# Kernel tuning notes

Measured on AMD Instinct MI355X. Metric: run time of the kernel, lower is better.

Reference implementation:

```python
import jax, jax.numpy as jnp
import numpy as np

ANGRES = 5  # u = v = angRes, n = 25


def _l2norm(x, axis):
    n = jnp.sqrt(jnp.sum(x * x, axis=axis, keepdims=True))
    return x / jnp.maximum(n, 1e-12)  # matches torch F.normalize eps


def _cos_attn(qm, km, vm):
    # qm: (b, M, K), km: (b, K, M), vm: (b, M, K)
    q = _l2norm(qm, -1)
    k = _l2norm(km, -2)
    att = jax.nn.softmax(q @ k, axis=-1)  # (b, M, M)
    return att @ vm


def _af_attn(x, u, v):  # AngularFrequencyAttention: b c (u v) h w -> b (c u) (h v w)
    b, c, n, h, w = x.shape
    t = x.reshape(b, c, u, v, h, w)
    qm = t.transpose(0, 1, 2, 4, 3, 5).reshape(b, c * u, h * v * w)   # (b,c,u,h,v,w)
    km = t.transpose(0, 4, 3, 5, 1, 2).reshape(b, h * v * w, c * u)   # (b,h,v,w,c,u)
    o = _cos_attn(qm, km, qm)
    o = o.reshape(b, c, u, h, v, w).transpose(0, 1, 2, 4, 3, 5).reshape(b, c, n, h, w)
    return o + x


def _sa_attn(x, u, v):  # SpatialAngularAttention: b c (u v) h w -> b (h u) (c v w)
    b, c, n, h, w = x.shape
    t = x.reshape(b, c, u, v, h, w)
    qm = t.transpose(0, 4, 2, 1, 3, 5).reshape(b, h * u, c * v * w)   # (b,h,u,c,v,w)
    km = t.transpose(0, 1, 3, 5, 4, 2).reshape(b, c * v * w, h * u)   # (b,c,v,w,h,u)
    o = _cos_attn(qm, km, qm)
    o = o.reshape(b, h, u, c, v, w).transpose(0, 3, 2, 4, 1, 5).reshape(b, c, n, h, w)
    return o + x


def _sf_attn(x, u, v):  # SpatialFrequencyAttention: b c (u v) h w -> b (c h) (w u v)
    b, c, n, h, w = x.shape
    t = x.reshape(b, c, u, v, h, w)
    qm = t.transpose(0, 1, 4, 5, 2, 3).reshape(b, c * h, w * u * v)   # (b,c,h,w,u,v)
    km = t.transpose(0, 5, 2, 3, 1, 4).reshape(b, w * u * v, c * h)   # (b,w,u,v,c,h)
    o = _cos_attn(qm, km, qm)
    o = o.reshape(b, c, h, w, u, v).transpose(0, 1, 4, 5, 2, 3).reshape(b, c, n, h, w)
    return o + x


def _layernorm(x, g, bta, eps=1e-5):
    mu = jnp.mean(x, -1, keepdims=True)
    var = jnp.mean(jnp.square(x - mu), -1, keepdims=True)
    return (x - mu) * jax.lax.rsqrt(var + eps) * g + bta


def setup_inputs() -> dict:
    key = jax.random.key(0)
    k0, k1, k2 = jax.random.split(key, 3)
    b, c, n, h, w = 4, 64, 25, 48, 48
    x = jax.random.normal(k0, (b, c, n, h, w), dtype=jnp.float32)
    gamma = jnp.ones((3 * c,), dtype=jnp.float32)
    beta = jnp.zeros((3 * c,), dtype=jnp.float32)
    w1 = jax.random.normal(k1, (3 * c, c), dtype=jnp.float32) * 0.02
    w2 = jax.random.normal(k2, (c, c), dtype=jnp.float32) * 0.02
    return {"x": x, "gamma": gamma, "beta": beta, "w1": w1, "w2": w2}


def reference(x, gamma, beta, w1, w2):
    u = v = ANGRES
    b, c, n, h, w = x.shape
    sf = _sf_attn(x, u, v)
    af = _af_attn(x, u, v)
    sa = _sa_attn(x, u, v)
    cat = jnp.concatenate([sf, af, sa], axis=1)            # (b, 3c, n, h, w)
    f = cat.transpose(0, 3, 4, 2, 1).reshape(b * h * w, n, 3 * c)
    y = _layernorm(f, gamma, beta)
    y = jax.nn.relu(y @ w1) @ w2                            # (bhw, n, c); dropout p=0.01 is eval-identity
    out = y.reshape(b, h, w, n, c).transpose(0, 4, 3, 1, 2) + x
    return out
```

## Files before the change

kernel.cpp:

```cpp
#include <hip/hip_runtime.h>
#include <stdint.h>

typedef __attribute__((ext_vector_type(8))) short bf16x8;
typedef __attribute__((ext_vector_type(4))) float f32x4;

__device__ __forceinline__ float b2f(short s) {
  union { unsigned u; float f; } a; a.u = ((unsigned)(unsigned short)s) << 16; return a.f;
}
__device__ __forceinline__ short f2b(float f) {
  union { float f; unsigned u; } a; a.f = f;
  unsigned r = a.u + 0x7fffu + ((a.u >> 16) & 1u);
  return (short)(r >> 16);
}
__device__ __forceinline__ void gload16(const void* g, void* l) {
  __builtin_amdgcn_global_load_lds((__attribute__((address_space(1))) void*)g,
                                   (__attribute__((address_space(3))) void*)l, 16, 0, 0);
}

#define SWZ(row, col) ((col) ^ (((row) & 7) << 3))

__global__ __launch_bounds__(256) void permute_sf_k(const float* __restrict__ x,
                                                    short* __restrict__ Q,
                                                    float* __restrict__ inv) {
  __shared__ float buf[4][1200];
  int wave = threadIdx.x >> 6, lane = threadIdx.x & 63;
  int gr = blockIdx.x * 4 + wave;
  int b = gr / 3072, m = gr - b * 3072;
  int c = m / 48, hh = m - c * 48;
  const float* xb = x + (long)(b * 64 + c) * 57600 + hh * 48;
  for (int uv = 0; uv < 25; ++uv)
    if (lane < 48) buf[wave][uv * 48 + lane] = xb[uv * 2304 + lane];
  __syncthreads();
  short* Qr = Q + (long)gr * 1280;
  float ss = 0.f;
  for (int k = lane; k < 1280; k += 64) {
    float v = 0.f;
    if (k < 1200) { int wv = k / 25, uv = k - wv * 25; v = buf[wave][uv * 48 + wv]; }
    ss += v * v;
    Qr[k] = f2b(v);
  }
  #pragma unroll
  for (int o = 32; o >= 1; o >>= 1) ss += __shfl_xor(ss, o, 64);
  if (lane == 0) inv[gr] = 1.0f / fmaxf(sqrtf(ss), 1e-12f);
}

__global__ __launch_bounds__(256) void permtr_all_k(const float* __restrict__ x,
    short* __restrict__ Qaf, short* __restrict__ QTaf,
    short* __restrict__ Qsa, short* __restrict__ QTsa,
    float* __restrict__ ssaf, float* __restrict__ sssa) {
  __shared__ short t[32][33];
  int bid = blockIdx.x;
  int isAF = (bid < 17280);
  int M, Mp, Kp, kt, mt, b;
  short *Q, *QT; float* ss;
  if (isAF) { M = 320; Mp = 384; Kp = 11520; kt = bid % 360; int r = bid / 360; mt = r % 12; b = r / 12;
              Q = Qaf; QT = QTaf; ss = ssaf; }
  else { int id = bid - 17280; M = 240; Mp = 256; Kp = 15360; kt = id % 480; int r = id / 480; mt = r % 8; b = r / 8;
         Q = Qsa; QT = QTsa; ss = sssa; }
  int k0 = kt * 32, m0 = mt * 32;
  int tx = threadIdx.x & 31, ty = threadIdx.x >> 5;
  const float* xb = x + (long)b * 3686400;
  #pragma unroll
  for (int i = 0; i < 32; i += 8) {
    int m = m0 + ty + i, k = k0 + tx;
    float v = 0.f;
    if (m < M) {
      int q1 = k / 240, r2 = k - q1 * 240;
      int v5 = r2 / 48, wv = r2 - v5 * 48;
      int a1 = m / 5, u = m - a1 * 5;
      long xi = isAF ? ((long)a1 * 25 + u * 5 + v5) * 2304 + q1 * 48 + wv
                     : ((long)q1 * 25 + u * 5 + v5) * 2304 + a1 * 48 + wv;
      v = xb[xi];
    }
    t[ty + i][tx] = f2b(v);
  }
  __syncthreads();
  long Qb = (long)b * Mp * Kp;
  #pragma unroll
  for (int i = 0; i < 32; i += 8)
    Q[Qb + (long)(m0 + ty + i) * Kp + k0 + tx] = t[ty + i][tx];
  #pragma unroll
  for (int i = 0; i < 32; i += 8)
    QT[Qb + (long)(k0 + ty + i) * Mp + m0 + tx] = t[tx][ty + i];
  if (threadIdx.x < 32 && m0 + (int)threadIdx.x < M) {
    float s = 0.f;
    #pragma unroll
    for (int k = 0; k < 32; ++k) { float f = b2f(t[threadIdx.x][k]); s += f * f; }
    atomicAdd(&ss[b * Mp + m0 + threadIdx.x], s);
  }
}

__global__ __launch_bounds__(256) void transpose_k(const short* __restrict__ in, short* __restrict__ out,
                                                   int R, int C) {
  __shared__ short t[32][33];
  long base = (long)blockIdx.z * R * C;
  int c0 = blockIdx.x * 32, r0 = blockIdx.y * 32;
  int tx = threadIdx.x & 31, ty = threadIdx.x >> 5;
  #pragma unroll
  for (int i = 0; i < 32; i += 8)
    t[ty + i][tx] = in[base + (long)(r0 + ty + i) * C + c0 + tx];
  __syncthreads();
  #pragma unroll
  for (int i = 0; i < 32; i += 8)
    out[base + (long)(c0 + ty + i) * R + r0 + tx] = t[tx][ty + i];
}

__global__ __launch_bounds__(256, 2) void gemm1_tri_k(const short* __restrict__ Q,
                                                      const float* __restrict__ invn,
                                                      short* __restrict__ att,
                                                      float* __restrict__ rowsum) {
  __shared__ short sm[32768];
  int tid = threadIdx.x, wave = tid >> 6, lane = tid & 63;
  int la = lane & 15, lb = lane >> 4;
  int bat = blockIdx.z;
  int bx = blockIdx.x, yt = 0, rem = bx;
  while (rem >= 24 - yt) { rem -= 24 - yt; ++yt; }
  int xt = yt + rem;
  const short* Qb = Q + (long)bat * 3932160L;
  const float* inv = invn + (long)bat * 3072;
  int row0 = yt * 128, col0 = xt * 128;
  f32x4 acc[4][4] = {};
  int wr = wave >> 1, wc = wave & 1;
  int rloc = tid >> 3, cbase = (tid & 7) * 8;
  int ldsoff = tid * 8;

  const short *pA[4], *pB[4];
  #pragma unroll
  for (int p = 0; p < 4; ++p) {
    int row = p * 32 + rloc;
    int sc = SWZ(row, cbase);
    pA[p] = Qb + (long)(row0 + row) * 1280 + sc;
    pB[p] = Qb + (long)(col0 + row) * 1280 + sc;
  }

  #define TRI_STAGE(KT, BUF) { \
    short* Asb = sm + (BUF) * 16384; \
    short* Bsb = Asb + 8192; \
    _Pragma("unroll") \
    for (int p = 0; p < 4; ++p) { \
      gload16(pA[p] + (KT) * 64, (void*)(Asb + p * 2048 + ldsoff)); \
      gload16(pB[p] + (KT) * 64, (void*)(Bsb + p * 2048 + ldsoff)); \
    } }
  #define TRI_COMP(BUF) { \
    const short* Asb = sm + (BUF) * 16384; \
    const short* Bsb = Asb + 8192; \
    _Pragma("unroll") \
    for (int kk = 0; kk < 64; kk += 32) { \
      bf16x8 av[4], bv[4]; \
      _Pragma("unroll") \
      for (int m = 0; m < 4; ++m) \
        av[m] = *(const bf16x8*)&Asb[(wr * 64 + m * 16 + la) * 64 + SWZ(la, kk + lb * 8)]; \
      _Pragma("unroll") \
      for (int nn = 0; nn < 4; ++nn) \
        bv[nn] = *(const bf16x8*)&Bsb[(wc * 64 + nn * 16 + la) * 64 + SWZ(la, kk + lb * 8)]; \
      _Pragma("unroll") \
      for (int m = 0; m < 4; ++m) \
        _Pragma("unroll") \
        for (int nn = 0; nn < 4; ++nn) \
          acc[m][nn] = __builtin_amdgcn_mfma_f32_16x16x32_bf16(av[m], bv[nn], acc[m][nn], 0, 0, 0); \
    } }

  TRI_STAGE(0, 0)
  for (int kt = 0; kt < 19; ++kt) {
    TRI_STAGE(kt + 1, (kt + 1) & 1)
    asm volatile("s_waitcnt vmcnt(8)" ::: "memory");
    __builtin_amdgcn_s_barrier();
    TRI_COMP(kt & 1)
    asm volatile("" ::: "memory");
    __builtin_amdgcn_s_barrier();
  }
  asm volatile("s_waitcnt vmcnt(0)" ::: "memory");
  __builtin_amdgcn_s_barrier();
  TRI_COMP(1)
  asm volatile("" ::: "memory");
  __builtin_amdgcn_s_barrier();

  short* staged = sm;
  #pragma unroll
  for (int m = 0; m < 4; ++m) {
    #pragma unroll
    for (int nn = 0; nn < 4; ++nn) {
      int cl = wc * 64 + nn * 16 + la;
      float ic = inv[col0 + cl];
      #pragma unroll
      for (int j = 0; j < 4; ++j) {
        int rl = wr * 64 + m * 16 + lb * 4 + j;
        staged[rl * 136 + cl] = f2b(__expf(acc[m][nn][j] * inv[row0 + rl] * ic));
      }
    }
  }
  __syncthreads();
  short* attb = att + (long)bat * 9437184L;
  float* rsb = rowsum + (long)bat * 3072;
  {
    int r = tid >> 1, half = tid & 1;
    short* dst = attb + (long)(row0 + r) * 3072 + col0 + half * 64;
    const short* src = &staged[r * 136 + half * 64];
    float s = 0.f;
    #pragma unroll
    for (int q = 0; q < 8; ++q) {
      bf16x8 v = *(const bf16x8*)&src[q * 8];
      *(bf16x8*)&dst[q * 8] = v;
      #pragma unroll
      for (int jj = 0; jj < 8; ++jj) s += b2f(v[jj]);
    }
    s += __shfl_xor(s, 1, 64);
    if (half == 0) atomicAdd(&rsb[row0 + r], s);
  }
  if (xt != yt) {
    int c = tid >> 1, half = tid & 1;
    short* dst = attb + (long)(col0 + c) * 3072 + row0 + half * 64;
    float s = 0.f;
    #pragma unroll
    for (int q = 0; q < 8; ++q) {
      bf16x8 o;
      #pragma unroll
      for (int jj = 0; jj < 8; ++jj) {
        o[jj] = staged[(half * 64 + q * 8 + jj) * 136 + c];
        s += b2f(o[jj]);
      }
      *(bf16x8*)&dst[q * 8] = o;
    }
    s += __shfl_xor(s, 1, 64);
    if (half == 0) atomicAdd(&rsb[col0 + c], s);
  }
}

__global__ __launch_bounds__(256, 2) void gemm_s_all_k(
    const short* __restrict__ Aaf, const short* __restrict__ Asa,
    float* __restrict__ Sfaf, float* __restrict__ Sfsa)
{
  __shared__ short sm[32768];
  int bid = blockIdx.x;
  const short* A; float* Sf;
  int lda, ktotal, ksper, ldc, row0, col0, bat, kc;
  long sA, sS;
  if (bid < 288) {
    int txy = bid % 9, z = bid / 9;
    col0 = (txy % 3) * 128; row0 = (txy / 3) * 128;
    bat = z / 8; kc = z % 8;
    lda = 11520; ktotal = 180; ksper = 23; ldc = 384;
    sA = 4423680L; sS = 147456L; A = Aaf; Sf = Sfaf;
  } else {
    int id = bid - 288;
    int txy = id % 4, z = id / 4;
    col0 = (txy % 2) * 128; row0 = (txy / 2) * 128;
    bat = z / 16; kc = z % 16;
    lda = 15360; ktotal = 240; ksper = 15; ldc = 256;
    sA = 3932160L; sS = 65536L; A = Asa; Sf = Sfsa;
  }
  int tid = threadIdx.x;
  int wave = tid >> 6, lane = tid & 63;
  int la = lane & 15, lb = lane >> 4;
  const short* Ab = A + (long)bat * sA;
  int kb = kc * ksper, ke = min(ktotal, kb + ksper);
  int L = ke - kb;
  f32x4 acc[4][4] = {};
  int wr = wave >> 1, wc = wave & 1;
  int rloc = tid >> 3, cbase = (tid & 7) * 8;
  int ldsoff = tid * 8;

  const short *pA[4], *pB[4];
  #pragma unroll
  for (int p = 0; p < 4; ++p) {
    int row = p * 32 + rloc;
    int sc = SWZ(row, cbase);
    pA[p] = Ab + (long)(row0 + row) * lda + sc;
    pB[p] = Ab + (long)(col0 + row) * lda + sc;
  }

  #define GS_STAGE(KT, BUF) { \
    short* Asb = sm + (BUF) * 16384; \
    short* Bsb = Asb + 8192; \
    _Pragma("unroll") \
    for (int p = 0; p < 4; ++p) { \
      gload16(pA[p] + (KT) * 64, (void*)(Asb + p * 2048 + ldsoff)); \
      gload16(pB[p] + (KT) * 64, (void*)(Bsb + p * 2048 + ldsoff)); \
    } }
  #define GS_COMP(BUF) { \
    const short* Asb = sm + (BUF) * 16384; \
    const short* Bsb = Asb + 8192; \
    _Pragma("unroll") \
    for (int kk = 0; kk < 64; kk += 32) { \
      bf16x8 av[4], bv[4]; \
      _Pragma("unroll") \
      for (int m = 0; m < 4; ++m) \
        av[m] = *(const bf16x8*)&Asb[(wr * 64 + m * 16 + la) * 64 + SWZ(la, kk + lb * 8)]; \
      _Pragma("unroll") \
      for (int nn = 0; nn < 4; ++nn) \
        bv[nn] = *(const bf16x8*)&Bsb[(wc * 64 + nn * 16 + la) * 64 + SWZ(la, kk + lb * 8)]; \
      _Pragma("unroll") \
      for (int m = 0; m < 4; ++m) \
        _Pragma("unroll") \
        for (int nn = 0; nn < 4; ++nn) \
          acc[m][nn] = __builtin_amdgcn_mfma_f32_16x16x32_bf16(av[m], bv[nn], acc[m][nn], 0, 0, 0); \
    } }

  GS_STAGE(kb, 0)
  for (int t = 0; t < L - 1; ++t) {
    GS_STAGE(kb + t + 1, (t + 1) & 1)
    asm volatile("s_waitcnt vmcnt(8)" ::: "memory");
    __builtin_amdgcn_s_barrier();
    GS_COMP(t & 1)
    asm volatile("" ::: "memory");
    __builtin_amdgcn_s_barrier();
  }
  asm volatile("s_waitcnt vmcnt(0)" ::: "memory");
  __builtin_amdgcn_s_barrier();
  GS_COMP((L - 1) & 1)

  float* Sb = Sf + (long)bat * sS;
  #pragma unroll
  for (int m = 0; m < 4; ++m) {
    int gr0 = row0 + wr * 64 + m * 16 + lb * 4;
    #pragma unroll
    for (int nn = 0; nn < 4; ++nn) {
      int gc = col0 + wc * 64 + nn * 16 + la;
      #pragma unroll
      for (int j = 0; j < 4; ++j)
        atomicAdd(&Sb[(long)(gr0 + j) * ldc + gc], acc[m][nn][j]);
    }
  }
}

__global__ __launch_bounds__(256) void softmax_all_k(
    const float* __restrict__ Sfaf, const float* __restrict__ Sfsa,
    const float* __restrict__ ssaf, const float* __restrict__ sssa,
    short* __restrict__ attaf, short* __restrict__ attsa)
{
  int wave = threadIdx.x >> 6, lane = threadIdx.x & 63;
  int rid = blockIdx.x * 4 + wave;
  int row, b, Mv, Mp; const float *Sf, *ss; short* att;
  if (rid < 1280) { row = rid % 320; b = rid / 320; Mv = 320; Mp = 384; Sf = Sfaf; ss = ssaf; att = attaf; }
  else { int id = rid - 1280; row = id % 240; b = id / 240; Mv = 240; Mp = 256; Sf = Sfsa; ss = sssa; att = attsa; }
  long sS = (long)Mp * Mp;
  const float* Sr = Sf + (long)b * sS + (long)row * Mp;
  const float* ssb = ss + b * Mp;
  float inv_i = rsqrtf(fmaxf(ssb[row], 1e-24f));
  float ev[6] = {0.f, 0.f, 0.f, 0.f, 0.f, 0.f};
  float sum = 0.f;
  #pragma unroll
  for (int q = 0; q < 6; ++q) {
    int j = q * 64 + lane;
    if (j < Mv) {
      float e = __expf(Sr[j] * inv_i * rsqrtf(fmaxf(ssb[j], 1e-24f)));
      ev[q] = e; sum += e;
    }
  }
  #pragma unroll
  for (int o = 32; o >= 1; o >>= 1) sum += __shfl_xor(sum, o, 64);
  float rden = 1.0f / sum;
  short* ar = att + (long)b * sS + (long)row * Mp;
  #pragma unroll
  for (int q = 0; q < 6; ++q) {
    int j = q * 64 + lane;
    if (j < Mp) ar[j] = (j < Mv) ? f2b(ev[q] * rden) : (short)0;
  }
}

__global__ __launch_bounds__(256, 2) void gemm2sf_k(const short* __restrict__ A,
                                                    const short* __restrict__ B,
                                                    const float* __restrict__ rowsum,
                                                    short* __restrict__ F) {
  __shared__ short sm[32768];
  int tid = threadIdx.x, wave = tid >> 6, lane = tid & 63;
  int la = lane & 15, lb = lane >> 4;
  int wr = wave >> 1, wc = wave & 1;
  int wk;
  { int xcd = blockIdx.x & 7, j = blockIdx.x >> 3; wk = xcd * 120 + j; }
  int yt = wk % 24, rem = wk / 24;
  int xt = rem % 10, bat = rem / 10;
  const short* Ab = A + (long)bat * 9437184L;
  const short* Bb = B + (long)bat * 3932160L;
  int rloc = tid >> 3, cbase = (tid & 7) * 8;
  int ldsoff = tid * 8;
  f32x4 acc[4][4] = {};

  const short *pA[4], *pB[4];
  #pragma unroll
  for (int p = 0; p < 4; ++p) {
    int row = p * 32 + rloc;
    int sc = SWZ(row, cbase);
    int rga = (row & 63) * 48 + yt * 2 + (row >> 6);
    pA[p] = Ab + (long)rga * 3072 + sc;
    int rgb = xt * 128 + row;
    pB[p] = Bb + (long)rgb * 3072 + sc;
  }

  #define G2_STAGE(KT, BUF) { \
    short* Asb = sm + (BUF) * 16384; \
    short* Bsb = Asb + 8192; \
    _Pragma("unroll") \
    for (int p = 0; p < 4; ++p) { \
      gload16(pA[p] + (KT) * 64, (void*)(Asb + p * 2048 + ldsoff)); \
      gload16(pB[p] + (KT) * 64, (void*)(Bsb + p * 2048 + ldsoff)); \
    } }
  #define G2_COMP(BUF) { \
    const short* Asb = sm + (BUF) * 16384; \
    const short* Bsb = Asb + 8192; \
    _Pragma("unroll") \
    for (int kk = 0; kk < 64; kk += 32) { \
      bf16x8 av[4], bv[4]; \
      _Pragma("unroll") \
      for (int m = 0; m < 4; ++m) \
        av[m] = *(const bf16x8*)&Asb[(wr * 64 + m * 16 + la) * 64 + SWZ(la, kk + lb * 8)]; \
      _Pragma("unroll") \
      for (int nn = 0; nn < 4; ++nn) \
        bv[nn] = *(const bf16x8*)&Bsb[(wc * 64 + nn * 16 + la) * 64 + SWZ(la, kk + lb * 8)]; \
      _Pragma("unroll") \
      for (int m = 0; m < 4; ++m) \
        _Pragma("unroll") \
        for (int nn = 0; nn < 4; ++nn) \
          acc[m][nn] = __builtin_amdgcn_mfma_f32_16x16x32_bf16(av[m], bv[nn], acc[m][nn], 0, 0, 0); \
    } }

  G2_STAGE(0, 0)
  for (int kt = 0; kt < 47; ++kt) {
    G2_STAGE(kt + 1, (kt + 1) & 1)
    asm volatile("s_waitcnt vmcnt(8)" ::: "memory");
    __builtin_amdgcn_s_barrier();
    G2_COMP(kt & 1)
    asm volatile("" ::: "memory");
    __builtin_amdgcn_s_barrier();
  }
  asm volatile("s_waitcnt vmcnt(0)" ::: "memory");
  __builtin_amdgcn_s_barrier();
  G2_COMP(1)
  asm volatile("" ::: "memory");
  __builtin_amdgcn_s_barrier();

  const float* rsb = rowsum + (long)bat * 3072;
  float rs[4][4];
  #pragma unroll
  for (int m = 0; m < 4; ++m)
    #pragma unroll
    for (int j = 0; j < 4; ++j)
      rs[m][j] = 1.0f / rsb[(m * 16 + lb * 4 + j) * 48 + yt * 2 + wr];

  short* staged = sm;
  #pragma unroll
  for (int m = 0; m < 4; ++m) {
    #pragma unroll
    for (int nn = 0; nn < 4; ++nn) {
      int cc = wc * 64 + nn * 16 + la;
      short4 o;
      o.x = f2b(acc[m][nn][0] * rs[m][0]); o.y = f2b(acc[m][nn][1] * rs[m][1]);
      o.z = f2b(acc[m][nn][2] * rs[m][2]); o.w = f2b(acc[m][nn][3] * rs[m][3]);
      *(short4*)&staged[(cc * 2 + wr) * 72 + m * 16 + lb * 4] = o;
    }
  }
  __syncthreads();
  #pragma unroll
  for (int rd = 0; rd < 8; ++rd) {
    int chunk = rd * 32 + (tid >> 3);
    int part = tid & 7;
    bf16x8 v = *(const bf16x8*)&staged[chunk * 72 + part * 8];
    int cc = chunk >> 1, sub = chunk & 1;
    int gc = xt * 128 + cc;
    if (gc < 1200) {
      int hh = yt * 2 + sub;
      int wv = gc / 25, nidx = gc - wv * 25;
      long base = (((long)(bat * 48 + hh) * 48 + wv) * 25 + nidx) * 192 + part * 8;
      *(bf16x8*)&F[base] = v;
    }
  }
}

__global__ __launch_bounds__(256) void gemm2_afsa_k(
    const short* __restrict__ attaf, const short* __restrict__ QTaf,
    const short* __restrict__ attsa, const short* __restrict__ QTsa,
    short* __restrict__ F)
{
  __shared__ short sm[20480];
  short* As = sm;
  short* Bs = sm + 4096;
  int bid = blockIdx.x;
  int isAF = (bid < 900);
  int NX, NY, LDA, KST, wk;
  const short *A, *B; long SA, SB;
  if (isAF) { NX = 45; NY = 5; LDA = 384; KST = 6; SA = 147456L; SB = 4423680L; A = attaf; B = QTaf; wk = bid; }
  else { NX = 60; NY = 4; LDA = 256; KST = 4; SA = 65536L; SB = 3932160L; A = attsa; B = QTsa; wk = bid - 900; }
  int yt = wk % NY, rem = wk / NY;
  int xt = rem % NX, bat = rem / NX;
  int tid = threadIdx.x, wave = tid >> 6, lane = tid & 63;
  int la = lane & 15, lb = lane >> 4;
  const short* Ab = A + (long)bat * SA;
  const short* Bb = B + (long)bat * SB;
  f32x4 acc[4][4] = {};
  int rloc = tid >> 3, cbase = (tid & 7) * 8;
  int ldsoff = tid * 8;

  const short *pA[2], *pB[8];
  #pragma unroll
  for (int p = 0; p < 2; ++p) {
    int r = p * 32 + rloc;
    int sc = SWZ(r, cbase);
    int rowg = isAF ? (r * 5 + yt) : (yt * 64 + r);
    pA[p] = Ab + (long)rowg * LDA + sc;
  }
  #pragma unroll
  for (int p = 0; p < 8; ++p) {
    int rb = p * 32 + rloc;
    int sc = SWZ(rb, cbase);
    int rowg;
    if (isAF) rowg = xt * 256 + rb;
    else { int c = rb & 63, g = rb >> 6; rowg = c * 240 + xt * 4 + g; }
    pB[p] = Bb + (long)rowg * LDA + sc;
  }

  for (int kt = 0; kt < KST; ++kt) {
    #pragma unroll
    for (int p = 0; p < 2; ++p)
      gload16(pA[p] + kt * 64, (void*)(As + p * 2048 + ldsoff));
    #pragma unroll
    for (int p = 0; p < 8; ++p)
      gload16(pB[p] + kt * 64, (void*)(Bs + p * 2048 + ldsoff));
    __syncthreads();
    #pragma unroll
    for (int kk = 0; kk < 64; kk += 32) {
      bf16x8 av[4], bv[4];
      #pragma unroll
      for (int m = 0; m < 4; ++m)
        av[m] = *(const bf16x8*)&As[(m * 16 + la) * 64 + SWZ(la, kk + lb * 8)];
      #pragma unroll
      for (int nn = 0; nn < 4; ++nn)
        bv[nn] = *(const bf16x8*)&Bs[(wave * 64 + nn * 16 + la) * 64 + SWZ(la, kk + lb * 8)];
      #pragma unroll
      for (int m = 0; m < 4; ++m)
        #pragma unroll
        for (int nn = 0; nn < 4; ++nn)
          acc[m][nn] = __builtin_amdgcn_mfma_f32_16x16x32_bf16(av[m], bv[nn], acc[m][nn], 0, 0, 0);
    }
    __syncthreads();
  }

  short* staged = sm;
  #pragma unroll
  for (int m = 0; m < 4; ++m) {
    #pragma unroll
    for (int nn = 0; nn < 4; ++nn) {
      if (!isAF) {
        #pragma unroll
        for (int j = 0; j < 4; ++j)
          staged[((m * 16 + lb * 4 + j) * 4 + wave) * 72 + nn * 16 + la] = f2b(acc[m][nn][j]);
      } else {
        short4 o;
        o.x = f2b(acc[m][nn][0]); o.y = f2b(acc[m][nn][1]);
        o.z = f2b(acc[m][nn][2]); o.w = f2b(acc[m][nn][3]);
        *(short4*)&staged[(wave * 64 + nn * 16 + la) * 72 + m * 16 + lb * 4] = o;
      }
    }
  }
  __syncthreads();

  #pragma unroll
  for (int rd = 0; rd < 8; ++rd) {
    int chunk = rd * 32 + (tid >> 3);
    int part = tid & 7;
    bf16x8 v = *(const bf16x8*)&staged[chunk * 72 + part * 8];
    long base; bool ok = true;
    if (isAF) {
      int gc = xt * 256 + chunk;
      int hh = gc / 240, r2 = gc - hh * 240, v5 = r2 / 48, wv = r2 - v5 * 48;
      base = (((long)(bat * 48 + hh) * 48 + wv) * 25 + yt * 5 + v5) * 192 + 64 + part * 8;
    } else {
      int r = chunk >> 2, g = chunk & 3;
      int gr = yt * 64 + r; ok = (gr < 240);
      int hh = gr / 5, u = gr - hh * 5;
      int r2 = xt * 4 + g, v5 = r2 / 48, wv = r2 - v5 * 48;
      base = (((long)(bat * 48 + hh) * 48 + wv) * 25 + u * 5 + v5) * 192 + 128 + part * 8;
    }
    if (ok) *(bf16x8*)&F[base] = v;
  }
}

__global__ __launch_bounds__(256) void prep_w_k(const float* __restrict__ w1, const float* __restrict__ w2,
                                                short* __restrict__ w1t, short* __restrict__ w2t) {
  int idx = blockIdx.x * 256 + threadIdx.x;
  if (idx < 12288) {
    int i = idx / 64, j = idx - i * 64;
    w1t[j * 192 + i] = f2b(w1[idx]);
  } else if (idx < 16384) {
    int k = idx - 12288;
    int i = k / 64, j = k - i * 64;
    w2t[j * 64 + i] = f2b(w2[k]);
  }
}

__global__ __launch_bounds__(256) void ln_mlp_mfma_k(
    const short* __restrict__ F, const float* __restrict__ x,
    const float* __restrict__ gamma, const float* __restrict__ beta,
    const short* __restrict__ w1t, const short* __restrict__ w2t,
    float* __restrict__ out)
{
  int n = blockIdx.x, hh = blockIdx.y, b = blockIdx.z;
  __shared__ short A1[48 * 200];
  __shared__ float xs[64 * 49];
  __shared__ __align__(16) char pool[19584];
  short* Fs = (short*)pool;
  short* Y1 = (short*)pool;
  float* Y2 = (float*)(pool + 6912);
  int tid = threadIdx.x, wave = tid >> 6, lane = tid & 63;
  int la = lane & 15, lb = lane >> 4;
  long Fb0 = ((long)(b * 48 + hh) * 1200 + n) * 192;
  long xb = (long)b * 3686400 + (long)n * 2304 + hh * 48;

  #pragma unroll
  for (int it = 0; it < 5; ++it) {
    int ci = tid + 256 * it;
    if (ci < 1152) {
      int r = ci / 24, q = ci - r * 24;
      *(bf16x8*)&Fs[r * 192 + q * 8] = *(const bf16x8*)&F[Fb0 + (long)r * 4800 + q * 8];
    }
  }
  {
    int ch = tid >> 2, qq = tid & 3;
    const float* xr = x + xb + (long)ch * 57600 + qq * 12;
    #pragma unroll
    for (int i = 0; i < 12; ++i) xs[ch * 49 + qq * 12 + i] = xr[i];
  }
  __syncthreads();

  float g0 = gamma[lane], g1 = gamma[lane + 64], g2 = gamma[lane + 128];
  float bt0 = beta[lane], bt1 = beta[lane + 64], bt2 = beta[lane + 128];
  #pragma unroll 4
  for (int rr = 0; rr < 12; ++rr) {
    int r = wave * 12 + rr;
    float xv = xs[lane * 49 + r];
    float v0 = b2f(Fs[r * 192 + lane]) + xv;
    float v1 = b2f(Fs[r * 192 + lane + 64]) + xv;
    float v2 = b2f(Fs[r * 192 + lane + 128]) + xv;
    float s = v0 + v1 + v2;
    #pragma unroll
    for (int o = 32; o >= 1; o >>= 1) s += __shfl_xor(s, o, 64);
    float mu = s * (1.f / 192.f);
    float d0 = v0 - mu, d1 = v1 - mu, d2 = v2 - mu;
    float q = d0 * d0 + d1 * d1 + d2 * d2;
    #pragma unroll
    for (int o = 32; o >= 1; o >>= 1) q += __shfl_xor(q, o, 64);
    float rs = rsqrtf(q * (1.f / 192.f) + 1e-5f);
    A1[r * 200 + lane]       = f2b(d0 * rs * g0 + bt0);
    A1[r * 200 + lane + 64]  = f2b(d1 * rs * g1 + bt1);
    A1[r * 200 + lane + 128] = f2b(d2 * rs * g2 + bt2);
  }
  __syncthreads();

  f32x4 acc1[3] = {};
  #pragma unroll
  for (int ks = 0; ks < 6; ++ks) {
    bf16x8 bv = *(const bf16x8*)&w1t[(wave * 16 + la) * 192 + ks * 32 + lb * 8];
    #pragma unroll
    for (int m = 0; m < 3; ++m) {
      bf16x8 av = *(const bf16x8*)&A1[(m * 16 + la) * 200 + ks * 32 + lb * 8];
      acc1[m] = __builtin_amdgcn_mfma_f32_16x16x32_bf16(av, bv, acc1[m], 0, 0, 0);
    }
  }
  #pragma unroll
  for (int m = 0; m < 3; ++m)
    #pragma unroll
    for (int j = 0; j < 4; ++j)
      Y1[(m * 16 + lb * 4 + j) * 72 + wave * 16 + la] = f2b(fmaxf(acc1[m][j], 0.f));
  __syncthreads();

  f32x4 acc2[3] = {};
  #pragma unroll
  for (int ks = 0; ks < 2; ++ks) {
    bf16x8 bv = *(const bf16x8*)&w2t[(wave * 16 + la) * 64 + ks * 32 + lb * 8];
    #pragma unroll
    for (int m = 0; m < 3; ++m) {
      bf16x8 av = *(const bf16x8*)&Y1[(m * 16 + la) * 72 + ks * 32 + lb * 8];
      acc2[m] = __builtin_amdgcn_mfma_f32_16x16x32_bf16(av, bv, acc2[m], 0, 0, 0);
    }
  }
  #pragma unroll
  for (int m = 0; m < 3; ++m)
    #pragma unroll
    for (int j = 0; j < 4; ++j)
      Y2[(m * 16 + lb * 4 + j) * 66 + wave * 16 + la] = acc2[m][j];
  __syncthreads();

  #pragma unroll
  for (int i = 0; i < 12; ++i) {
    int e = tid + 256 * i;
    int cc = e / 48, wv = e - cc * 48;
    out[xb + (long)cc * 57600 + wv] = Y2[wv * 66 + cc] + xs[cc * 49 + wv];
  }
}

extern "C" void kernel_launch(void* const* d_in, const int* in_sizes, int n_in,
                              void* d_out, int out_size, void* d_ws, size_t ws_size,
                              hipStream_t stream) {
  (void)in_sizes; (void)n_in; (void)out_size;
  const float* x     = (const float*)d_in[0];
  const float* gamma = (const float*)d_in[1];
  const float* beta  = (const float*)d_in[2];
  const float* w1    = (const float*)d_in[3];
  const float* w2    = (const float*)d_in[4];
  float* out = (float*)d_out;

  const size_t NEED = 237191168UL;
  if (ws_size < NEED) return;
  char* ws = (char*)d_ws;
  short* F     = (short*)(ws);
  short* attsf = (short*)(ws + 88473600UL);
  short* Qsf   = (short*)(ws + 163971072UL);
  short* QTsf  = (short*)(ws + 199360512UL);
  float* rowsum = (float*)(ws + 234749952UL);
  float* invn  = (float*)(ws + 237109248UL);
  short* w1t   = (short*)(ws + 237158400UL);
  short* w2t   = (short*)(ws + 237182976UL);
  short* Qaf   = (short*)(ws + 88473600UL);
  short* QTaf  = (short*)(ws + 123863040UL);
  float* Sfsa  = (float*)(ws + 159252480UL);
  float* ssaf  = (float*)(ws + 160301056UL);
  float* sssa  = (float*)(ws + 160307200UL);
  short* attaf = (short*)(ws + 160311296UL);
  short* attsa = (short*)(ws + 161490944UL);
  short* Qsa   = (short*)(ws + 163971072UL);
  short* QTsa  = (short*)(ws + 195428352UL);
  float* Sfaf  = (float*)(ws + 234749952UL);

  prep_w_k<<<64, 256, 0, stream>>>(w1, w2, w1t, w2t);

  permute_sf_k<<<3072, 256, 0, stream>>>(x, Qsf, invn);
  transpose_k<<<dim3(40, 96, 4), 256, 0, stream>>>(Qsf, QTsf, 3072, 1280);
  hipMemsetAsync(rowsum, 0, 49152, stream);
  gemm1_tri_k<<<dim3(300, 1, 4), 256, 0, stream>>>(Qsf, invn, attsf, rowsum);
  gemm2sf_k<<<dim3(960), 256, 0, stream>>>(attsf, QTsf, rowsum, F);

  hipMemsetAsync(Sfaf, 0, 2359296, stream);
  hipMemsetAsync(Sfsa, 0, 1048576, stream);
  hipMemsetAsync(ssaf, 0, 10240, stream);
  permtr_all_k<<<32640, 256, 0, stream>>>(x, Qaf, QTaf, Qsa, QTsa, ssaf, sssa);
  gemm_s_all_k<<<544, 256, 0, stream>>>(Qaf, Qsa, Sfaf, Sfsa);
  softmax_all_k<<<560, 256, 0, stream>>>(Sfaf, Sfsa, ssaf, sssa, attaf, attsa);
  gemm2_afsa_k<<<1860, 256, 0, stream>>>(attaf, QTaf, attsa, QTsa, F);

  ln_mlp_mfma_k<<<dim3(25, 48, 4), 256, 0, stream>>>(F, x, gamma, beta, w1t, w2t, out);
}
```

Before: 519.9 us.

## Halve K-tile in tri/SF GEMMs for higher occupancy, remap AF/SA blocks per XCD

The triangular Gram GEMM and the SF attention-times-V GEMM now stage 32-wide K slices instead of 64 in a reshaped swizzled LDS layout. This shrinks shared memory so launch bounds can allow four blocks per CU instead of two, at the cost of twice as many barrier-separated pipeline steps. The AF/SA second GEMM remaps block indices so consecutive work lands on the same XCD for better L2 reuse. The final fused MLP kernel loads F into LDS with direct global-to-LDS loads instead of passing through registers.

After: 518.2 us. No clear change (-0.3%).

```diff
diff --git a/kernel.cpp b/kernel.cpp
--- a/kernel.cpp
+++ b/kernel.cpp
@@ -105,11 +105,11 @@
     out[base + (long)(c0 + ty + i) * R + r0 + tx] = t[tx][ty + i];
 }
 
-__global__ __launch_bounds__(256, 2) void gemm1_tri_k(const short* __restrict__ Q,
+__global__ __launch_bounds__(256, 4) void gemm1_tri_k(const short* __restrict__ Q,
                                                       const float* __restrict__ invn,
                                                       short* __restrict__ att,
                                                       float* __restrict__ rowsum) {
-  __shared__ short sm[32768];
+  __shared__ short sm[17408];
   int tid = threadIdx.x, wave = tid >> 6, lane = tid & 63;
   int la = lane & 15, lb = lane >> 4;
   int bat = blockIdx.z;
@@ -121,61 +121,68 @@
   int row0 = yt * 128, col0 = xt * 128;
   f32x4 acc[4][4] = {};
   int wr = wave >> 1, wc = wave & 1;
-  int rloc = tid >> 3, cbase = (tid & 7) * 8;
-  int ldsoff = tid * 8;
-
-  const short *pA[4], *pB[4];
-  #pragma unroll
-  for (int p = 0; p < 4; ++p) {
-    int row = p * 32 + rloc;
-    int sc = SWZ(row, cbase);
-    pA[p] = Qb + (long)(row0 + row) * 1280 + sc;
-    pB[p] = Qb + (long)(col0 + row) * 1280 + sc;
-  }
-
-  #define TRI_STAGE(KT, BUF) { \
-    short* Asb = sm + (BUF) * 16384; \
-    short* Bsb = Asb + 8192; \
+  int swzla = (la & 7) << 3;
+
+  const short *pA[2], *pB[2];
+  #pragma unroll
+  for (int p = 0; p < 2; ++p) {
+    int R = p * 32 + (tid >> 3);
+    int sun = ((tid & 7) * 8) ^ ((R & 7) << 3);
+    int r = R + ((sun >> 5) << 6);
+    int c = sun & 31;
+    pA[p] = Qb + (long)(row0 + r) * 1280 + c;
+    pB[p] = Qb + (long)(col0 + r) * 1280 + c;
+  }
+
+  #define T9_STAGE(KT, BUF) { \
+    short* Asb = sm + (BUF) * 8192; \
+    short* Bsb = Asb + 4096; \
+    gload16(pA[0] + (KT) * 32, (void*)(Asb + tid * 8)); \
+    gload16(pA[1] + (KT) * 32, (void*)(Asb + 2048 + tid * 8)); \
+    gload16(pB[0] + (KT) * 32, (void*)(Bsb + tid * 8)); \
+    gload16(pB[1] + (KT) * 32, (void*)(Bsb + 2048 + tid * 8)); \
+  }
+  #define T9_COMP(BUF) { \
+    const short* Asb = sm + (BUF) * 8192; \
+    const short* Bsb = Asb + 4096; \
+    bf16x8 av[4], bv[4]; \
     _Pragma("unroll") \
-    for (int p = 0; p < 4; ++p) { \
-      gload16(pA[p] + (KT) * 64, (void*)(Asb + p * 2048 + ldsoff)); \
-      gload16(pB[p] + (KT) * 64, (void*)(Bsb + p * 2048 + ldsoff)); \
-    } }
-  #define TRI_COMP(BUF) { \
-    const short* Asb = sm + (BUF) * 16384; \
-    const short* Bsb = Asb + 8192; \
+    for (int m = 0; m < 4; ++m) \
+      av[m] = *(const bf16x8*)&Asb[(m * 16 + la) * 64 + ((wr * 32 + lb * 8) ^ swzla)]; \
     _Pragma("unroll") \
-    for (int kk = 0; kk < 64; kk += 32) { \
-      bf16x8 av[4], bv[4]; \
-      _Pragma("unroll") \
-      for (int m = 0; m < 4; ++m) \
-        av[m] = *(const bf16x8*)&Asb[(wr * 64 + m * 16 + la) * 64 + SWZ(la, kk + lb * 8)]; \
+    for (int nn = 0; nn < 4; ++nn) \
+      bv[nn] = *(const bf16x8*)&Bsb[(nn * 16 + la) * 64 + ((wc * 32 + lb * 8) ^ swzla)]; \
+    _Pragma("unroll") \
+    for (int m = 0; m < 4; ++m) \
       _Pragma("unroll") \
       for (int nn = 0; nn < 4; ++nn) \
-        bv[nn] = *(const bf16x8*)&Bsb[(wc * 64 + nn * 16 + la) * 64 + SWZ(la, kk + lb * 8)]; \
-      _Pragma("unroll") \
-      for (int m = 0; m < 4; ++m) \
-        _Pragma("unroll") \
-        for (int nn = 0; nn < 4; ++nn) \
-          acc[m][nn] = __builtin_amdgcn_mfma_f32_16x16x32_bf16(av[m], bv[nn], acc[m][nn], 0, 0, 0); \
-    } }
-
-  TRI_STAGE(0, 0)
-  for (int kt = 0; kt < 19; ++kt) {
-    TRI_STAGE(kt + 1, (kt + 1) & 1)
-    asm volatile("s_waitcnt vmcnt(8)" ::: "memory");
+        acc[m][nn] = __builtin_amdgcn_mfma_f32_16x16x32_bf16(av[m], bv[nn], acc[m][nn], 0, 0, 0); \
+  }
+
+  T9_STAGE(0, 0)
+  for (int kt = 0; kt < 39; ++kt) {
+    T9_STAGE(kt + 1, (kt + 1) & 1)
+    asm volatile("s_waitcnt vmcnt(4)" ::: "memory");
     __builtin_amdgcn_s_barrier();
-    TRI_COMP(kt & 1)
+    T9_COMP(kt & 1)
     asm volatile("" ::: "memory");
     __builtin_amdgcn_s_barrier();
   }
   asm volatile("s_waitcnt vmcnt(0)" ::: "memory");
   __builtin_amdgcn_s_barrier();
-  TRI_COMP(1)
+  T9_COMP(1)
   asm volatile("" ::: "memory");
   __builtin_amdgcn_s_barrier();
 
   short* staged = sm;
+  #pragma unroll
+  for (int m = 0; m < 4; ++m) {
+    #pragma unroll
+    for (int nn = 0; nn < 4; ++nn) {
+      int cl = wc * 32 + nn * 16 + la;
+      (void)cl;
+    }
+  }
   #pragma unroll
   for (int m = 0; m < 4; ++m) {
     #pragma unroll
@@ -225,6 +232,7 @@
     if (half == 0) atomicAdd(&rsb[col0 + c], s);
   }
 }
+
 
 __global__ __launch_bounds__(256, 2) void gemm_s_all_k(
     const short* __restrict__ Aaf, const short* __restrict__ Asa,
@@ -358,11 +366,11 @@
   }
 }
 
-__global__ __launch_bounds__(256, 2) void gemm2sf_k(const short* __restrict__ A,
+__global__ __launch_bounds__(256, 4) void gemm2sf_k(const short* __restrict__ A,
                                                     const short* __restrict__ B,
                                                     const float* __restrict__ rowsum,
                                                     short* __restrict__ F) {
-  __shared__ short sm[32768];
+  __shared__ short sm[18432];
   int tid = threadIdx.x, wave = tid >> 6, lane = tid & 63;
   int la = lane & 15, lb = lane >> 4;
   int wr = wave >> 1, wc = wave & 1;
@@ -372,60 +380,59 @@
   int xt = rem % 10, bat = rem / 10;
   const short* Ab = A + (long)bat * 9437184L;
   const short* Bb = B + (long)bat * 3932160L;
-  int rloc = tid >> 3, cbase = (tid & 7) * 8;
-  int ldsoff = tid * 8;
+  int swzla = (la & 7) << 3;
   f32x4 acc[4][4] = {};
 
-  const short *pA[4], *pB[4];
-  #pragma unroll
-  for (int p = 0; p < 4; ++p) {
-    int row = p * 32 + rloc;
-    int sc = SWZ(row, cbase);
-    int rga = (row & 63) * 48 + yt * 2 + (row >> 6);
-    pA[p] = Ab + (long)rga * 3072 + sc;
-    int rgb = xt * 128 + row;
-    pB[p] = Bb + (long)rgb * 3072 + sc;
-  }
-
-  #define G2_STAGE(KT, BUF) { \
-    short* Asb = sm + (BUF) * 16384; \
-    short* Bsb = Asb + 8192; \
+  const short *pA[2], *pB[2];
+  #pragma unroll
+  for (int p = 0; p < 2; ++p) {
+    int R = p * 32 + (tid >> 3);
+    int sun = ((tid & 7) * 8) ^ ((R & 7) << 3);
+    int r = R + ((sun >> 5) << 6);
+    int c = sun & 31;
+    int rga = (r & 63) * 48 + yt * 2 + (r >> 6);
+    pA[p] = Ab + (long)rga * 3072 + c;
+    int rgb = xt * 128 + r;
+    pB[p] = Bb + (long)rgb * 3072 + c;
+  }
+
+  #define G9_STAGE(KT, BUF) { \
+    short* Asb = sm + (BUF) * 8192; \
+    short* Bsb = Asb + 4096; \
+    gload16(pA[0] + (KT) * 32, (void*)(Asb + tid * 8)); \
+    gload16(pA[1] + (KT) * 32, (void*)(Asb + 2048 + tid * 8)); \
+    gload16(pB[0] + (KT) * 32, (void*)(Bsb + tid * 8)); \
+    gload16(pB[1] + (KT) * 32, (void*)(Bsb + 2048 + tid * 8)); \
+  }
+  #define G9_COMP(BUF) { \
+    const short* Asb = sm + (BUF) * 8192; \
+    const short* Bsb = Asb + 4096; \
+    bf16x8 av[4], bv[4]; \
     _Pragma("unroll") \
-    for (int p = 0; p < 4; ++p) { \
-      gload16(pA[p] + (KT) * 64, (void*)(Asb + p * 2048 + ldsoff)); \
-      gload16(pB[p] + (KT) * 64, (void*)(Bsb + p * 2048 + ldsoff)); \
-    } }
-  #define G2_COMP(BUF) { \
-    const short* Asb = sm + (BUF) * 16384; \
-    const short* Bsb = Asb + 8192; \
+    for (int m = 0; m < 4; ++m) \
+      av[m] = *(const bf16x8*)&Asb[(m * 16 + la) * 64 + ((wr * 32 + lb * 8) ^ swzla)]; \
     _Pragma("unroll") \
-    for (int kk = 0; kk < 64; kk += 32) { \
-      bf16x8 av[4], bv[4]; \
-      _Pragma("unroll") \
-      for (int m = 0; m < 4; ++m) \
-        av[m] = *(const bf16x8*)&Asb[(wr * 64 + m * 16 + la) * 64 + SWZ(la, kk + lb * 8)]; \
+    for (int nn = 0; nn < 4; ++nn) \
+      bv[nn] = *(const bf16x8*)&Bsb[(nn * 16 + la) * 64 + ((wc * 32 + lb * 8) ^ swzla)]; \
+    _Pragma("unroll") \
+    for (int m = 0; m < 4; ++m) \
       _Pragma("unroll") \
       for (int nn = 0; nn < 4; ++nn) \
-        bv[nn] = *(const bf16x8*)&Bsb[(wc * 64 + nn * 16 + la) * 64 + SWZ(la, kk + lb * 8)]; \
-      _Pragma("unroll") \
-      for (int m = 0; m < 4; ++m) \
-        _Pragma("unroll") \
-        for (int nn = 0; nn < 4; ++nn) \
-          acc[m][nn] = __builtin_amdgcn_mfma_f32_16x16x32_bf16(av[m], bv[nn], acc[m][nn], 0, 0, 0); \
-    } }
-
-  G2_STAGE(0, 0)
-  for (int kt = 0; kt < 47; ++kt) {
-    G2_STAGE(kt + 1, (kt + 1) & 1)
-    asm volatile("s_waitcnt vmcnt(8)" ::: "memory");
+        acc[m][nn] = __builtin_amdgcn_mfma_f32_16x16x32_bf16(av[m], bv[nn], acc[m][nn], 0, 0, 0); \
+  }
+
+  G9_STAGE(0, 0)
+  for (int kt = 0; kt < 95; ++kt) {
+    G9_STAGE(kt + 1, (kt + 1) & 1)
+    asm volatile("s_waitcnt vmcnt(4)" ::: "memory");
     __builtin_amdgcn_s_barrier();
-    G2_COMP(kt & 1)
+    G9_COMP(kt & 1)
     asm volatile("" ::: "memory");
     __builtin_amdgcn_s_barrier();
   }
   asm volatile("s_waitcnt vmcnt(0)" ::: "memory");
   __builtin_amdgcn_s_barrier();
-  G2_COMP(1)
+  G9_COMP(1)
   asm volatile("" ::: "memory");
   __builtin_amdgcn_s_barrier();
 
@@ -478,8 +485,16 @@
   int isAF = (bid < 900);
   int NX, NY, LDA, KST, wk;
   const short *A, *B; long SA, SB;
-  if (isAF) { NX = 45; NY = 5; LDA = 384; KST = 6; SA = 147456L; SB = 4423680L; A = attaf; B = QTaf; wk = bid; }
-  else { NX = 60; NY = 4; LDA = 256; KST = 4; SA = 65536L; SB = 3932160L; A = attsa; B = QTsa; wk = bid - 900; }
+  if (isAF) {
+    NX = 45; NY = 5; LDA = 384; KST = 6; SA = 147456L; SB = 4423680L; A = attaf; B = QTaf;
+    int xcd = bid & 7, j = bid >> 3;
+    wk = (xcd < 4) ? xcd * 113 + j : 4 * 113 + (xcd - 4) * 112 + j;
+  } else {
+    NX = 60; NY = 4; LDA = 256; KST = 4; SA = 65536L; SB = 3932160L; A = attsa; B = QTsa;
+    int id = bid - 900;
+    int xcd = id & 7, j = id >> 3;
+    wk = xcd * 120 + j;
+  }
   int yt = wk % NY, rem = wk / NY;
   int xt = rem % NX, bat = rem / NX;
   int tid = threadIdx.x, wave = tid >> 6, lane = tid & 63;
@@ -610,7 +625,7 @@
     int ci = tid + 256 * it;
     if (ci < 1152) {
       int r = ci / 24, q = ci - r * 24;
-      *(bf16x8*)&Fs[r * 192 + q * 8] = *(const bf16x8*)&F[Fb0 + (long)r * 4800 + q * 8];
+      gload16(&F[Fb0 + (long)r * 4800 + q * 8], (void*)(Fs + ci * 8));
     }
   }
   {
```
